# Kernel tuning notes

Measured on AMD Instinct MI355X. Metric: run time of the kernel, lower is better.

Reference implementation:

```python
import jax, jax.numpy as jnp
import numpy as np

N = 50000          # nodes
E = 800000         # edges (avg degree 16)
IN = 128           # input feature dim
HID = 64           # hidden dim per head
HEADS = 2          # attention heads (all but last layer)
OUT = 64           # out_dim (last layer, 1 head)
NC = 2             # num_classes
NEG_SLOPE = 0.2    # dgl GATConv leaky_relu slope


def setup_inputs() -> dict:
    key = jax.random.key(0)
    ks = jax.random.split(key, 20)
    rn = lambda k, shape, s=0.05: (jax.random.normal(k, shape, jnp.float32) * s)
    W_IO = HID * HEADS  # 128, width between GAT layers
    return {
        "x": rn(ks[0], (N, IN), 1.0),
        "src": jax.random.randint(ks[1], (E,), 0, N, dtype=jnp.int32),
        "dst": jax.random.randint(ks[2], (E,), 0, N, dtype=jnp.int32),
        # embedding_h: Linear(IN, HID*HEADS)
        "W_emb": rn(ks[3], (IN, W_IO)),
        "b_emb": jnp.zeros((W_IO,), jnp.float32),
        # GAT layer 0: in 128 -> 2 heads x 64
        "W0": rn(ks[4], (W_IO, HEADS * HID)),
        "al0": rn(ks[5], (HEADS, HID)),
        "ar0": rn(ks[6], (HEADS, HID)),
        "b0": jnp.zeros((HEADS * HID,), jnp.float32),
        # GAT layer 1: in 128 -> 2 heads x 64
        "W1": rn(ks[7], (W_IO, HEADS * HID)),
        "al1": rn(ks[8], (HEADS, HID)),
        "ar1": rn(ks[9], (HEADS, HID)),
        "b1": jnp.zeros((HEADS * HID,), jnp.float32),
        # GAT layer 2 (last): in 128 -> 1 head x OUT
        "W2": rn(ks[10], (W_IO, 1 * OUT)),
        "al2": rn(ks[11], (1, OUT)),
        "ar2": rn(ks[12], (1, OUT)),
        "b2": jnp.zeros((OUT,), jnp.float32),
        # edge scorer: Linear(2*OUT, NC)
        "Ws": rn(ks[13], (2 * OUT, NC)),
        "bs": jnp.zeros((NC,), jnp.float32),
    }


def gat_layer(h, src, dst, W, al, ar, b):
    """dgl GATConv + elu (GATLayer with batch_norm=False, residual=False)."""
    heads, out = al.shape
    feat = (h @ W).reshape(-1, heads, out)            # [N,H,D]
    el = jnp.sum(feat * al, axis=-1)                  # [N,H]
    er = jnp.sum(feat * ar, axis=-1)                  # [N,H]
    e = jax.nn.leaky_relu(el[src] + er[dst], NEG_SLOPE)  # [E,H]
    # edge softmax over incoming edges of each dst node
    emax = jax.ops.segment_max(e, dst, num_segments=N)   # [N,H]
    ex = jnp.exp(e - emax[dst])                          # [E,H]
    denom = jax.ops.segment_sum(ex, dst, num_segments=N) # [N,H]
    alpha = ex / jnp.where(denom[dst] > 0, denom[dst], 1.0)
    msg = feat[src] * alpha[:, :, None]                  # [E,H,D]
    rst = jax.ops.segment_sum(msg, dst, num_segments=N)  # [N,H,D]
    rst = rst.reshape(-1, heads * out) + b
    return jax.nn.elu(rst)


def reference(x, W_emb, b_emb, W0, al0, ar0, b0, W1, al1, ar1, b1,
              W2, al2, ar2, b2, Ws, bs, src, dst):
    h = x @ W_emb + b_emb                    # embedding_h (dropout p -> eval/identity)
    h = gat_layer(h, src, dst, W0, al0, ar0, b0)
    h = gat_layer(h, src, dst, W1, al1, ar1, b1)
    h = gat_layer(h, src, dst, W2, al2, ar2, b2)   # [N, OUT]
    # edge scorer on the scored subgraph: concat(src_h, dst_h) -> Linear
    he = jnp.concatenate([h[src], h[dst]], axis=1)  # [E, 2*OUT]
    return he @ Ws + bs                             # [E, NC]
```

## Files before the change

### kernel.cpp

```cpp
#include <hip/hip_runtime.h>
#include <hip/hip_bf16.h>
#include <math.h>


constexpr float SLOPE = 0.2f;

__device__ __forceinline__ float b2f(unsigned short u) {
  union { unsigned int i; float f; } v;
  v.i = ((unsigned int)u) << 16;
  return v.f;
}
__device__ __forceinline__ unsigned short f2b(float f) {
  unsigned int x = __float_as_uint(f);
  unsigned int r = (x + 0x7fffu + ((x >> 16) & 1u)) >> 16;
  return (unsigned short)r;
}

template<int M, bool OUTBF16>
__global__ __launch_bounds__(512)
void gemm_k128(const float* __restrict__ X, const float* __restrict__ W,
               const float* __restrict__ bias,
               const float* __restrict__ al, const float* __restrict__ ar,
               void* __restrict__ Yv, float* __restrict__ el,
               float* __restrict__ er, int N) {
  constexpr int K = 128;
  constexpr int BM = 64;
  constexpr int CPT = M / 32;
  constexpr int H = M / 64;
  constexpr int WH4 = (64 * M) / 4;
  __shared__ __align__(16) float Xs[BM][K];
  __shared__ __align__(16) float Wsm[64][M];

  const int tid = threadIdx.x;
  const int row0 = blockIdx.x * BM;

  #pragma unroll
  for (int j = 0; j < (BM * K) / (512 * 4); ++j) {
    int lin = tid + j * 512;
    int r = lin >> 5;
    int c4 = lin & 31;
    int gr = row0 + r;
    float4 v = make_float4(0.f, 0.f, 0.f, 0.f);
    if (gr < N) v = reinterpret_cast<const float4*>(X + (size_t)gr * K)[c4];
    reinterpret_cast<float4*>(&Xs[r][0])[c4] = v;
  }
  #pragma unroll
  for (int j = 0; j < WH4 / 512; ++j) {
    int lin = tid + j * 512;
    reinterpret_cast<float4*>(&Wsm[0][0])[lin] =
        reinterpret_cast<const float4*>(W)[lin];
  }
  __syncthreads();

  const int tr = tid >> 5;
  const int tc = tid & 31;

  float acc[4][CPT];
  #pragma unroll
  for (int i = 0; i < 4; ++i)
    #pragma unroll
    for (int c = 0; c < CPT; ++c) acc[i][c] = 0.f;

  #pragma unroll
  for (int half = 0; half < 2; ++half) {
    #pragma unroll 2
    for (int k4l = 0; k4l < 16; ++k4l) {
      const int kg = half * 64 + k4l * 4;
      float4 xv[4];
      #pragma unroll
      for (int i = 0; i < 4; ++i)
        xv[i] = *reinterpret_cast<const float4*>(&Xs[tr * 4 + i][kg]);
      if constexpr (CPT == 4) {
        float4 wv[4];
        #pragma unroll
        for (int kk = 0; kk < 4; ++kk)
          wv[kk] = *reinterpret_cast<const float4*>(&Wsm[k4l * 4 + kk][tc * 4]);
        #pragma unroll
        for (int i = 0; i < 4; ++i) {
          const float* xp = reinterpret_cast<const float*>(&xv[i]);
          #pragma unroll
          for (int kk = 0; kk < 4; ++kk) {
            acc[i][0] += xp[kk] * wv[kk].x;
            acc[i][1] += xp[kk] * wv[kk].y;
            acc[i][2] += xp[kk] * wv[kk].z;
            acc[i][3] += xp[kk] * wv[kk].w;
          }
        }
      } else {
        float2 wv[4];
        #pragma unroll
        for (int kk = 0; kk < 4; ++kk)
          wv[kk] = *reinterpret_cast<const float2*>(&Wsm[k4l * 4 + kk][tc * 2]);
        #pragma unroll
        for (int i = 0; i < 4; ++i) {
          const float* xp = reinterpret_cast<const float*>(&xv[i]);
          #pragma unroll
          for (int kk = 0; kk < 4; ++kk) {
            acc[i][0] += xp[kk] * wv[kk].x;
            acc[i][1] += xp[kk] * wv[kk].y;
          }
        }
      }
    }
    if (half == 0) {
      __syncthreads();
      #pragma unroll
      for (int j = 0; j < WH4 / 512; ++j) {
        int lin = tid + j * 512;
        reinterpret_cast<float4*>(&Wsm[0][0])[lin] =
            reinterpret_cast<const float4*>(W)[WH4 + lin];
      }
      __syncthreads();
    }
  }

  float bv[CPT];
  #pragma unroll
  for (int c = 0; c < CPT; ++c) bv[c] = bias ? bias[tc * CPT + c] : 0.f;

  #pragma unroll
  for (int i = 0; i < 4; ++i) {
    int gr = row0 + tr * 4 + i;
    if (gr < N) {
      if constexpr (OUTBF16) {
        unsigned short* Yb = reinterpret_cast<unsigned short*>(Yv);
        if constexpr (CPT == 4) {
          ushort4 o;
          o.x = f2b(acc[i][0] + bv[0]);
          o.y = f2b(acc[i][1] + bv[1]);
          o.z = f2b(acc[i][2] + bv[2]);
          o.w = f2b(acc[i][3] + bv[3]);
          *reinterpret_cast<ushort4*>(&Yb[(size_t)gr * M + tc * 4]) = o;
        } else {
          ushort2 o;
          o.x = f2b(acc[i][0] + bv[0]);
          o.y = f2b(acc[i][1] + bv[1]);
          *reinterpret_cast<ushort2*>(&Yb[(size_t)gr * M + tc * 2]) = o;
        }
      } else {
        float* Y = reinterpret_cast<float*>(Yv);
        if constexpr (CPT == 4) {
          float4 o = make_float4(acc[i][0] + bv[0], acc[i][1] + bv[1],
                                 acc[i][2] + bv[2], acc[i][3] + bv[3]);
          *reinterpret_cast<float4*>(&Y[(size_t)gr * M + tc * 4]) = o;
        } else {
          float2 o = make_float2(acc[i][0] + bv[0], acc[i][1] + bv[1]);
          *reinterpret_cast<float2*>(&Y[(size_t)gr * M + tc * 2]) = o;
        }
      }
    }
  }

  if (al != nullptr) {
    int head, colbase;
    if constexpr (CPT == 4) { head = tc >> 4; colbase = tc * 4 - head * 64; }
    else                    { head = 0;       colbase = tc * 2; }
    float av[CPT], rv[CPT];
    #pragma unroll
    for (int c = 0; c < CPT; ++c) {
      av[c] = al[head * 64 + colbase + c];
      rv[c] = ar[head * 64 + colbase + c];
    }
    #pragma unroll
    for (int i = 0; i < 4; ++i) {
      float pl = 0.f, pr = 0.f;
      #pragma unroll
      for (int c = 0; c < CPT; ++c) {
        pl += acc[i][c] * av[c];
        pr += acc[i][c] * rv[c];
      }
      if constexpr (CPT == 4) {
        #pragma unroll
        for (int off = 1; off < 16; off <<= 1) {
          pl += __shfl_xor(pl, off);
          pr += __shfl_xor(pr, off);
        }
        if ((tc & 15) == 0) {
          int gr = row0 + tr * 4 + i;
          if (gr < N) { el[gr * H + head] = pl; er[gr * H + head] = pr; }
        }
      } else {
        #pragma unroll
        for (int off = 1; off < 32; off <<= 1) {
          pl += __shfl_xor(pl, off);
          pr += __shfl_xor(pr, off);
        }
        if (tc == 0) {
          int gr = row0 + tr * 4 + i;
          if (gr < N) { el[gr] = pl; er[gr] = pr; }
        }
      }
    }
  }
}

__global__ void count_dst(const int* __restrict__ dst, int* __restrict__ cnt,
                          int E) {
  int i = blockIdx.x * blockDim.x + threadIdx.x;
  if (i < E) atomicAdd(&cnt[dst[i]], 1);
}

__global__ void scan1(const int* __restrict__ cnt, int* __restrict__ outv,
                      int* __restrict__ bsum, int n) {
  __shared__ int sm[256];
  int tid = threadIdx.x;
  int base = blockIdx.x * 1024 + tid * 4;
  int pre[4];
  int s = 0;
  #pragma unroll
  for (int j = 0; j < 4; ++j) {
    int idx = base + j;
    int v = (idx < n) ? cnt[idx] : 0;
    pre[j] = s;
    s += v;
  }
  sm[tid] = s;
  __syncthreads();
  for (int off = 1; off < 256; off <<= 1) {
    int a = (tid >= off) ? sm[tid - off] : 0;
    __syncthreads();
    sm[tid] += a;
    __syncthreads();
  }
  int excl = sm[tid] - s;
  #pragma unroll
  for (int j = 0; j < 4; ++j) {
    int idx = base + j;
    if (idx < n) outv[idx] = excl + pre[j];
  }
  if (tid == 255) bsum[blockIdx.x] = sm[255];
}

__global__ void scan2(const int* __restrict__ bsum, int* __restrict__ btop,
                      int nb, int* __restrict__ row_last) {
  if (threadIdx.x == 0 && blockIdx.x == 0) {
    int s = 0;
    for (int i = 0; i < nb; ++i) { btop[i] = s; s += bsum[i]; }
    *row_last = s;
  }
}

__global__ void scan3(int* __restrict__ rp, int* __restrict__ cur,
                      const int* __restrict__ btop, int n) {
  int i = blockIdx.x * blockDim.x + threadIdx.x;
  if (i < n) {
    int v = rp[i] + btop[i >> 10];
    rp[i] = v;
    cur[i] = v;
  }
}

__global__ void scatter_edges(const int* __restrict__ src,
                              const int* __restrict__ dst,
                              int* __restrict__ cur,
                              int* __restrict__ s_csr,
                              int* __restrict__ d_csr, int E) {
  int i = blockIdx.x * blockDim.x + threadIdx.x;
  if (i < E) {
    int d = dst[i];
    int p = atomicAdd(&cur[d], 1);
    s_csr[p] = src[i];
    d_csr[p] = d;
  }
}

template<int H>
__global__ void edge_prep(const int* __restrict__ s_csr,
                          const int* __restrict__ d_csr,
                          const float* __restrict__ el,
                          const float* __restrict__ er,
                          float2* __restrict__ edat, int E) {
  int i = blockIdx.x * blockDim.x + threadIdx.x;
  if (i >= E) return;
  int s = s_csr[i];
  int d = d_csr[i];
  float sb = __int_as_float(s);
  if constexpr (H == 2) {
    float2 le = reinterpret_cast<const float2*>(el)[s];
    float2 re = reinterpret_cast<const float2*>(er)[d];
    float e0 = le.x + re.x;
    float e1 = le.y + re.y;
    e0 = e0 > 0.f ? e0 : SLOPE * e0;
    e1 = e1 > 0.f ? e1 : SLOPE * e1;
    edat[i] = make_float2(__expf(e0), sb);
    edat[(size_t)E + i] = make_float2(__expf(e1), sb);
  } else {
    float ev = el[s] + er[d];
    ev = ev > 0.f ? ev : SLOPE * ev;
    edat[i] = make_float2(__expf(ev), sb);
  }
}

template<int H, bool SCORE>
__global__ __launch_bounds__(256)
void gat_aggregate(const unsigned short* __restrict__ featb,
                   const float2* __restrict__ edat,
                   const float* __restrict__ bias,
                   const int* __restrict__ row_ptr,
                   float* __restrict__ hout,
                   const float* __restrict__ Wsc,
                   float* __restrict__ ps, float* __restrict__ pd,
                   int N, int E) {
  int tid = threadIdx.x;
  int pid = blockIdx.x * 16 + (tid >> 4);
  int sl = tid & 15;
  const int NH = N * H;
  bool live = pid < NH;
  int pc = live ? pid : 0;
  int node, head;
  if constexpr (H == 2) { node = pc >> 1; head = pc & 1; }
  else                  { node = pc;      head = 0; }
  int beg = live ? row_ptr[node] : 0;
  int end = live ? row_ptr[node + 1] : 0;

  const int rowoff = head * 64 + sl * 4;
  const float2* edath = edat + (size_t)head * E;

  float4 acc = make_float4(0.f, 0.f, 0.f, 0.f);
  float den = 0.f;

  for (int p = beg; p < end; p += 8) {
    #pragma unroll
    for (int j = 0; j < 8; ++j) {
      int q = p + j;
      int qc = q < end ? q : end - 1;
      float2 ed = edath[qc];
      float ex = q < end ? ed.x : 0.f;
      int s = __float_as_int(ed.y);
      ushort4 u = *reinterpret_cast<const ushort4*>(
          &featb[(size_t)s * (H * 64) + rowoff]);
      den += ex;
      acc.x += ex * b2f(u.x);
      acc.y += ex * b2f(u.y);
      acc.z += ex * b2f(u.z);
      acc.w += ex * b2f(u.w);
    }
  }

  if (live) {
    float inv = 1.f / (den > 0.f ? den : 1.f);
    float4 bv = reinterpret_cast<const float4*>(bias)[head * 16 + sl];
    float4 r;
    r.x = acc.x * inv + bv.x;
    r.y = acc.y * inv + bv.y;
    r.z = acc.z * inv + bv.z;
    r.w = acc.w * inv + bv.w;
    r.x = r.x > 0.f ? r.x : expm1f(r.x);
    r.y = r.y > 0.f ? r.y : expm1f(r.y);
    r.z = r.z > 0.f ? r.z : expm1f(r.z);
    r.w = r.w > 0.f ? r.w : expm1f(r.w);

    if constexpr (!SCORE) {
      reinterpret_cast<float4*>(hout)[(size_t)pid * 16 + sl] = r;
    } else {
      float s0 = r.x * Wsc[(4 * sl + 0) * 2] + r.y * Wsc[(4 * sl + 1) * 2] +
                 r.z * Wsc[(4 * sl + 2) * 2] + r.w * Wsc[(4 * sl + 3) * 2];
      float s1 = r.x * Wsc[(4 * sl + 0) * 2 + 1] + r.y * Wsc[(4 * sl + 1) * 2 + 1] +
                 r.z * Wsc[(4 * sl + 2) * 2 + 1] + r.w * Wsc[(4 * sl + 3) * 2 + 1];
      float d0 = r.x * Wsc[(64 + 4 * sl + 0) * 2] + r.y * Wsc[(64 + 4 * sl + 1) * 2] +
                 r.z * Wsc[(64 + 4 * sl + 2) * 2] + r.w * Wsc[(64 + 4 * sl + 3) * 2];
      float d1 = r.x * Wsc[(64 + 4 * sl + 0) * 2 + 1] + r.y * Wsc[(64 + 4 * sl + 1) * 2 + 1] +
                 r.z * Wsc[(64 + 4 * sl + 2) * 2 + 1] + r.w * Wsc[(64 + 4 * sl + 3) * 2 + 1];
      #pragma unroll
      for (int off = 1; off < 16; off <<= 1) {
        s0 += __shfl_xor(s0, off);
        s1 += __shfl_xor(s1, off);
        d0 += __shfl_xor(d0, off);
        d1 += __shfl_xor(d1, off);
      }
      if (sl == 0) {
        ps[node * 2 + 0] = s0;
        ps[node * 2 + 1] = s1;
        pd[node * 2 + 0] = d0;
        pd[node * 2 + 1] = d1;
      }
    }
  }
}

__global__ void score_out(const int* __restrict__ src,
                          const int* __restrict__ dst,
                          const float* __restrict__ ps,
                          const float* __restrict__ pd,
                          const float* __restrict__ bs,
                          float* __restrict__ out, int E) {
  int i = blockIdx.x * blockDim.x + threadIdx.x;
  if (i < E) {
    int s = src[i], d = dst[i];
    float2 a = *reinterpret_cast<const float2*>(ps + (size_t)s * 2);
    float2 b = *reinterpret_cast<const float2*>(pd + (size_t)d * 2);
    float2 o;
    o.x = a.x + b.x + bs[0];
    o.y = a.y + b.y + bs[1];
    *reinterpret_cast<float2*>(out + (size_t)i * 2) = o;
  }
}

extern "C" void kernel_launch(void* const* d_in, const int* in_sizes, int n_in,
                              void* d_out, int out_size, void* d_ws,
                              size_t ws_size, hipStream_t stream) {
  const float* x    = (const float*)d_in[0];
  const int*   src  = (const int*)d_in[1];
  const int*   dst  = (const int*)d_in[2];
  const float* Wemb = (const float*)d_in[3];
  const float* bemb = (const float*)d_in[4];
  const float* W0   = (const float*)d_in[5];
  const float* al0  = (const float*)d_in[6];
  const float* ar0  = (const float*)d_in[7];
  const float* b0   = (const float*)d_in[8];
  const float* W1   = (const float*)d_in[9];
  const float* al1  = (const float*)d_in[10];
  const float* ar1  = (const float*)d_in[11];
  const float* b1   = (const float*)d_in[12];
  const float* W2   = (const float*)d_in[13];
  const float* al2  = (const float*)d_in[14];
  const float* ar2  = (const float*)d_in[15];
  const float* b2   = (const float*)d_in[16];
  const float* Wsc  = (const float*)d_in[17];
  const float* bsc  = (const float*)d_in[18];

  const int N = in_sizes[0] / 128;
  const int E = in_sizes[1];
  float* out = (float*)d_out;

  char* w = (char*)d_ws;
  float*  A    = (float*)w;  w += (size_t)N * 128 * 4;
  float2* edat = (float2*)w; w += (size_t)E * 2 * 8;
  unsigned short* Bb = (unsigned short*)w; w += (size_t)N * 128 * 2;
  float* el  = (float*)w; w += (size_t)N * 2 * 4;
  float* er  = (float*)w; w += (size_t)N * 2 * 4;
  float* ps  = (float*)w; w += (size_t)N * 2 * 4;
  float* pd  = (float*)w; w += (size_t)N * 2 * 4;
  int* s_csr = (int*)w;   w += (size_t)E * 4;
  int* d_csr = (int*)w;   w += (size_t)E * 4;
  int* cnt   = (int*)w;   w += (size_t)N * 4;
  int* rp    = (int*)w;   w += (size_t)(N + 4) * 4;
  int* cur   = (int*)w;   w += (size_t)N * 4;
  int* bsum  = (int*)w;   w += 4096;
  int* btop  = (int*)w;   w += 4096;

  hipMemsetAsync(cnt, 0, (size_t)N * 4, stream);
  count_dst<<<(E + 255) / 256, 256, 0, stream>>>(dst, cnt, E);
  int nb = (N + 1023) / 1024;
  scan1<<<nb, 256, 0, stream>>>(cnt, rp, bsum, N);
  scan2<<<1, 64, 0, stream>>>(bsum, btop, nb, rp + N);
  scan3<<<(N + 255) / 256, 256, 0, stream>>>(rp, cur, btop, N);
  scatter_edges<<<(E + 255) / 256, 256, 0, stream>>>(src, dst, cur, s_csr,
                                                     d_csr, E);

  const int gb = (N + 63) / 64;
  const int eb = (E + 255) / 256;
  const int pb2 = (N * 2 + 15) / 16;
  const int pb1 = (N * 1 + 15) / 16;

  gemm_k128<128, false><<<gb, 512, 0, stream>>>(x, Wemb, bemb, nullptr, nullptr,
                                                A, nullptr, nullptr, N);

  gemm_k128<128, true><<<gb, 512, 0, stream>>>(A, W0, nullptr, al0, ar0,
                                               Bb, el, er, N);
  edge_prep<2><<<eb, 256, 0, stream>>>(s_csr, d_csr, el, er, edat, E);
  gat_aggregate<2, false><<<pb2, 256, 0, stream>>>(Bb, edat, b0, rp, A,
                                                   nullptr, nullptr, nullptr,
                                                   N, E);
  gemm_k128<128, true><<<gb, 512, 0, stream>>>(A, W1, nullptr, al1, ar1,
                                               Bb, el, er, N);
  edge_prep<2><<<eb, 256, 0, stream>>>(s_csr, d_csr, el, er, edat, E);
  gat_aggregate<2, false><<<pb2, 256, 0, stream>>>(Bb, edat, b1, rp, A,
                                                   nullptr, nullptr, nullptr,
                                                   N, E);
  gemm_k128<64, true><<<gb, 512, 0, stream>>>(A, W2, nullptr, al2, ar2,
                                              Bb, el, er, N);
  edge_prep<1><<<eb, 256, 0, stream>>>(s_csr, d_csr, el, er, edat, E);
  gat_aggregate<1, true><<<pb1, 256, 0, stream>>>(Bb, edat, b2, rp, nullptr,
                                                  Wsc, ps, pd, N, E);

  score_out<<<(E + 255) / 256, 256, 0, stream>>>(src, dst, ps, pd, bsc, out, E);
}
```

Measured before the change: 444.6 us.

## Build CSR via two-pass bucketed scatter and node-parallel edge prep

Replaces the single atomic scatter of edges into CSR with a two-stage scheme. Edges are first bucketed into groups of 16 destination nodes using coarse atomics, then each bucket is finalized by one block whose atomics hit a small, cache-local region. Edge prep now walks the CSR per destination node, so the d_csr array is no longer needed and er is loaded once per node. This trades an extra pass and an E-sized temp buffer for better write locality and fewer scattered accesses.

```diff
diff --git a/kernel.cpp b/kernel.cpp
--- a/kernel.cpp
+++ b/kernel.cpp
@@ -241,53 +241,77 @@
 }
 
 __global__ void scan3(int* __restrict__ rp, int* __restrict__ cur,
-                      const int* __restrict__ btop, int n) {
+                      int* __restrict__ bcur, const int* __restrict__ btop,
+                      int n) {
   int i = blockIdx.x * blockDim.x + threadIdx.x;
   if (i < n) {
     int v = rp[i] + btop[i >> 10];
     rp[i] = v;
     cur[i] = v;
-  }
-}
-
-__global__ void scatter_edges(const int* __restrict__ src,
-                              const int* __restrict__ dst,
-                              int* __restrict__ cur,
-                              int* __restrict__ s_csr,
-                              int* __restrict__ d_csr, int E) {
+    if ((i & 15) == 0) bcur[i >> 4] = v;
+  }
+}
+
+__global__ void bucket_scatter(const int* __restrict__ src,
+                               const int* __restrict__ dst,
+                               int* __restrict__ bcur,
+                               int2* __restrict__ tmp, int E) {
   int i = blockIdx.x * blockDim.x + threadIdx.x;
   if (i < E) {
     int d = dst[i];
-    int p = atomicAdd(&cur[d], 1);
-    s_csr[p] = src[i];
-    d_csr[p] = d;
+    int p = atomicAdd(&bcur[d >> 4], 1);
+    tmp[p] = make_int2(src[i], d);
+  }
+}
+
+__global__ void final_scatter(const int2* __restrict__ tmp,
+                              const int* __restrict__ rp,
+                              int* __restrict__ cur,
+                              int* __restrict__ s_csr, int N) {
+  int b = blockIdx.x;
+  int n0 = b << 4;
+  int n1 = n0 + 16; if (n1 > N) n1 = N;
+  int beg = rp[n0];
+  int end = rp[n1];
+  for (int p = beg + threadIdx.x; p < end; p += blockDim.x) {
+    int2 e = tmp[p];
+    int q = atomicAdd(&cur[e.y], 1);
+    s_csr[q] = e.x;
   }
 }
 
 template<int H>
-__global__ void edge_prep(const int* __restrict__ s_csr,
-                          const int* __restrict__ d_csr,
-                          const float* __restrict__ el,
-                          const float* __restrict__ er,
-                          float2* __restrict__ edat, int E) {
-  int i = blockIdx.x * blockDim.x + threadIdx.x;
-  if (i >= E) return;
-  int s = s_csr[i];
-  int d = d_csr[i];
-  float sb = __int_as_float(s);
+__global__ __launch_bounds__(256)
+void edge_prep(const int* __restrict__ s_csr, const float* __restrict__ el,
+               const float* __restrict__ er, const int* __restrict__ rp,
+               float2* __restrict__ edat, int N, int E) {
+  int tid = threadIdx.x;
+  int node = blockIdx.x * 16 + (tid >> 4);
+  int sl = tid & 15;
+  if (node >= N) return;
+  int beg = rp[node];
+  int end = rp[node + 1];
   if constexpr (H == 2) {
-    float2 le = reinterpret_cast<const float2*>(el)[s];
-    float2 re = reinterpret_cast<const float2*>(er)[d];
-    float e0 = le.x + re.x;
-    float e1 = le.y + re.y;
-    e0 = e0 > 0.f ? e0 : SLOPE * e0;
-    e1 = e1 > 0.f ? e1 : SLOPE * e1;
-    edat[i] = make_float2(__expf(e0), sb);
-    edat[(size_t)E + i] = make_float2(__expf(e1), sb);
+    float2 re = reinterpret_cast<const float2*>(er)[node];
+    for (int p = beg + sl; p < end; p += 16) {
+      int s = s_csr[p];
+      float2 le = reinterpret_cast<const float2*>(el)[s];
+      float e0 = le.x + re.x;
+      float e1 = le.y + re.y;
+      e0 = e0 > 0.f ? e0 : SLOPE * e0;
+      e1 = e1 > 0.f ? e1 : SLOPE * e1;
+      float sb = __int_as_float(s);
+      edat[p] = make_float2(__expf(e0), sb);
+      edat[(size_t)E + p] = make_float2(__expf(e1), sb);
+    }
   } else {
-    float ev = el[s] + er[d];
-    ev = ev > 0.f ? ev : SLOPE * ev;
-    edat[i] = make_float2(__expf(ev), sb);
+    float re = er[node];
+    for (int p = beg + sl; p < end; p += 16) {
+      int s = s_csr[p];
+      float ev = el[s] + re;
+      ev = ev > 0.f ? ev : SLOPE * ev;
+      edat[p] = make_float2(__expf(ev), __int_as_float(s));
+    }
   }
 }
 
@@ -422,20 +446,22 @@
   const int N = in_sizes[0] / 128;
   const int E = in_sizes[1];
   float* out = (float*)d_out;
+  const int NB = (N + 15) / 16;
 
   char* w = (char*)d_ws;
   float*  A    = (float*)w;  w += (size_t)N * 128 * 4;
   float2* edat = (float2*)w; w += (size_t)E * 2 * 8;
+  int2*   tmp  = (int2*)w;   w += (size_t)E * 8;
   unsigned short* Bb = (unsigned short*)w; w += (size_t)N * 128 * 2;
   float* el  = (float*)w; w += (size_t)N * 2 * 4;
   float* er  = (float*)w; w += (size_t)N * 2 * 4;
   float* ps  = (float*)w; w += (size_t)N * 2 * 4;
   float* pd  = (float*)w; w += (size_t)N * 2 * 4;
   int* s_csr = (int*)w;   w += (size_t)E * 4;
-  int* d_csr = (int*)w;   w += (size_t)E * 4;
   int* cnt   = (int*)w;   w += (size_t)N * 4;
   int* rp    = (int*)w;   w += (size_t)(N + 4) * 4;
   int* cur   = (int*)w;   w += (size_t)N * 4;
+  int* bcur  = (int*)w;   w += (size_t)NB * 4;
   int* bsum  = (int*)w;   w += 4096;
   int* btop  = (int*)w;   w += 4096;
 
@@ -444,12 +470,12 @@
   int nb = (N + 1023) / 1024;
   scan1<<<nb, 256, 0, stream>>>(cnt, rp, bsum, N);
   scan2<<<1, 64, 0, stream>>>(bsum, btop, nb, rp + N);
-  scan3<<<(N + 255) / 256, 256, 0, stream>>>(rp, cur, btop, N);
-  scatter_edges<<<(E + 255) / 256, 256, 0, stream>>>(src, dst, cur, s_csr,
-                                                     d_csr, E);
+  scan3<<<(N + 255) / 256, 256, 0, stream>>>(rp, cur, bcur, btop, N);
+  bucket_scatter<<<(E + 255) / 256, 256, 0, stream>>>(src, dst, bcur, tmp, E);
+  final_scatter<<<NB, 256, 0, stream>>>(tmp, rp, cur, s_csr, N);
 
   const int gb = (N + 63) / 64;
-  const int eb = (E + 255) / 256;
+  const int nbk = (N + 15) / 16;
   const int pb2 = (N * 2 + 15) / 16;
   const int pb1 = (N * 1 + 15) / 16;
 
@@ -458,19 +484,19 @@
 
   gemm_k128<128, true><<<gb, 512, 0, stream>>>(A, W0, nullptr, al0, ar0,
                                                Bb, el, er, N);
-  edge_prep<2><<<eb, 256, 0, stream>>>(s_csr, d_csr, el, er, edat, E);
+  edge_prep<2><<<nbk, 256, 0, stream>>>(s_csr, el, er, rp, edat, N, E);
   gat_aggregate<2, false><<<pb2, 256, 0, stream>>>(Bb, edat, b0, rp, A,
                                                    nullptr, nullptr, nullptr,
                                                    N, E);
   gemm_k128<128, true><<<gb, 512, 0, stream>>>(A, W1, nullptr, al1, ar1,
                                                Bb, el, er, N);
-  edge_prep<2><<<eb, 256, 0, stream>>>(s_csr, d_csr, el, er, edat, E);
+  edge_prep<2><<<nbk, 256, 0, stream>>>(s_csr, el, er, rp, edat, N, E);
   gat_aggregate<2, false><<<pb2, 256, 0, stream>>>(Bb, edat, b1, rp, A,
                                                    nullptr, nullptr, nullptr,
                                                    N, E);
   gemm_k128<64, true><<<gb, 512, 0, stream>>>(A, W2, nullptr, al2, ar2,
                                               Bb, el, er, N);
-  edge_prep<1><<<eb, 256, 0, stream>>>(s_csr, d_csr, el, er, edat, E);
+  edge_prep<1><<<nbk, 256, 0, stream>>>(s_csr, el, er, rp, edat, N, E);
   gat_aggregate<1, true><<<pb1, 256, 0, stream>>>(Bb, edat, b2, rp, nullptr,
                                                   Wsc, ps, pd, N, E);
 
```

Result: slower. 503.0 us (+13.1%).
